# Kernel tuning notes

Hardware: AMD Instinct MI355X
Metric: run time of the kernel (lower is better)

The kernel has to match this reference:

```python
import jax, jax.numpy as jnp
import numpy as np

T, B, F_, H, D, C = 16, 1024, 512, 128, 8, 100  # trees, batch, feat, hidden, depth, classes
L = 2 ** (D + 1)  # n_leaf = 512


def _routing_tables():
    # Static per-leaf routing: node index and branch side at each depth.
    # Derived from compute_mu's gather indices:
    #   node(d, l) = 2^d - 1 + l // 2^(D+1-d);  side(d, l) = (l // 2^(D-d)) % 2
    l = np.arange(L)
    node = np.stack([(2 ** d - 1) + l // (2 ** (D + 1 - d)) for d in range(D + 1)])  # [D+1, L]
    side = np.stack([(l // (2 ** (D - d))) % 2 for d in range(D + 1)])               # [D+1, L]
    return jnp.asarray(node, dtype=jnp.int32), jnp.asarray(side.astype(np.bool_))


def setup_inputs() -> dict:
    key = jax.random.key(0)
    ks = jax.random.split(key, 4)
    return {
        "feat": jax.random.normal(ks[0], (B, F_), jnp.float32),
        "W1": jax.random.normal(ks[1], (T, F_, H), jnp.float32) * 0.05,
        "b1": jnp.zeros((T, H), jnp.float32),
        "W2": jax.random.normal(ks[2], (T, H, L), jnp.float32) * 0.05,
        "b2": jnp.zeros((T, L), jnp.float32),
        "pi": jax.random.uniform(ks[3], (T, L, C), jnp.float32, -2.0, 2.0),
    }


def reference(feat, W1, b1, W2, b2, pi):
    node, side = _routing_tables()
    # Per-tree MLP head (dropout is identity in eval mode).
    h = jax.nn.relu(jnp.einsum('bf,tfh->tbh', feat, W1) + b1[:, None, :])        # [T,B,H]
    p = jax.nn.sigmoid(jnp.einsum('tbh,thl->tbl', h, W2) + b2[:, None, :])       # [T,B,L]
    # compute_mu: product of routing probs along each root->leaf path.
    sel = p[:, :, node]                          # [T,B,D+1,L] gather (static indices)
    route = jnp.where(side, 1.0 - sel, sel)      # left -> p, right -> 1-p
    mu = jnp.prod(route, axis=2)                 # [T,B,L]
    # compute_py_x: mean over leaves then mean over trees of mu @ softmax(pi).
    leaf_p = jax.nn.softmax(pi, axis=-1)         # [T,L,C]
    py_x = jnp.einsum('tbl,tlc->bc', mu, leaf_p) / (L * T)  # [B,C]
    return jnp.log(py_x)
```

## Files before the change

### kernel.cpp

```cpp
#include <hip/hip_runtime.h>
#include <hip/hip_bf16.h>
#include <math.h>

#define T_ 16
#define B_ 1024
#define F_ 512
#define H_ 128
#define D_ 8
#define C_ 100
#define L_ 512
#define CPAD 128

typedef __attribute__((ext_vector_type(8))) short bf16x8_t;
typedef __attribute__((ext_vector_type(4))) float f32x4_t;

__device__ inline ushort f2bf(float x) {
  __hip_bfloat16 b = __float2bfloat16(x);
  return *(ushort*)&b;
}
__device__ inline float bf2f(ushort u) {
  union { unsigned int i; float f; } v;
  v.i = ((unsigned int)u) << 16;
  return v.f;
}

__global__ __launch_bounds__(256) void k_prep(
    const float* __restrict__ feat, const float* __restrict__ W1,
    const float* __restrict__ W2, const float* __restrict__ pi,
    ushort* __restrict__ feat_bf, ushort* __restrict__ W1T,
    ushort* __restrict__ W2T, ushort* __restrict__ lpT) {
  __shared__ ushort sm[8320];
  const int bid = blockIdx.x, tid = threadIdx.x;

  if (bid < 256) {
    int i = (bid * 256 + tid) * 8;
    float4 a = *(const float4*)(feat + i);
    float4 b = *(const float4*)(feat + i + 4);
    bf16x8_t o;
    o[0] = (short)f2bf(a.x); o[1] = (short)f2bf(a.y);
    o[2] = (short)f2bf(a.z); o[3] = (short)f2bf(a.w);
    o[4] = (short)f2bf(b.x); o[5] = (short)f2bf(b.y);
    o[6] = (short)f2bf(b.z); o[7] = (short)f2bf(b.w);
    *(bf16x8_t*)(feat_bf + i) = o;
    return;
  }
  if (bid < 2304) {
    float (*tile)[33] = (float(*)[33])sm;
    const float* X; ushort* XT; int K, N, kb, nb, s;
    if (bid < 1280) {
      int r = bid - 256;  kb = r & 15; nb = (r >> 4) & 3;  s = r >> 6;
      X = W1; XT = W1T; K = F_; N = H_;
    } else {
      int r = bid - 1280; kb = r & 3;  nb = (r >> 2) & 15; s = r >> 6;
      X = W2; XT = W2T; K = H_; N = L_;
    }
    const int k0 = kb * 32, n0 = nb * 32;
    const int c = tid & 31, r0 = tid >> 5;
    const float* Xs = X + (size_t)s * K * N;
    ushort* XTs = XT + (size_t)s * N * K;
#pragma unroll
    for (int j = 0; j < 4; ++j)
      tile[r0 + 8 * j][c] = Xs[(size_t)(k0 + r0 + 8 * j) * N + n0 + c];
    __syncthreads();
#pragma unroll
    for (int j = 0; j < 4; ++j)
      XTs[(size_t)(n0 + r0 + 8 * j) * K + k0 + c] = f2bf(tile[c][r0 + 8 * j]);
    return;
  }
  {
    ushort (*ts)[130] = (ushort(*)[130])sm;
    const int idx = bid - 2304;
    const int R0 = idx * 64;
    const int t = R0 >> 9, li0 = R0 & 511;
    const int wave = tid >> 6, lane = tid & 63;
    for (int it = 0; it < 16; ++it) {
      int r = wave * 16 + it;
      const float* x = pi + (size_t)(R0 + r) * C_;
      float v0 = (lane < C_) ? x[lane] : -1e30f;
      float v1 = (lane + 64 < C_) ? x[lane + 64] : -1e30f;
      float m = fmaxf(v0, v1);
#pragma unroll
      for (int off = 32; off; off >>= 1) m = fmaxf(m, __shfl_xor(m, off, 64));
      float e0 = __expf(v0 - m);
      float e1 = (lane + 64 < C_) ? __expf(v1 - m) : 0.0f;
      float s = e0 + e1;
#pragma unroll
      for (int off = 32; off; off >>= 1) s += __shfl_xor(s, off, 64);
      float inv = 1.0f / s;
      ts[r][lane]      = (lane < C_) ? f2bf(e0 * inv) : (ushort)0;
      ts[r][lane + 64] = (lane + 64 < C_) ? f2bf(e1 * inv) : (ushort)0;
    }
    __syncthreads();
    int c = tid >> 1, hf = tid & 1;
    ushort tmp[32];
#pragma unroll
    for (int j = 0; j < 32; ++j) tmp[j] = ts[hf * 32 + j][c];
    ushort* dst = lpT + ((size_t)t * CPAD + c) * L_ + li0 + hf * 32;
#pragma unroll
    for (int j = 0; j < 4; ++j)
      *(bf16x8_t*)(dst + 8 * j) = *(bf16x8_t*)&tmp[8 * j];
  }
}

__global__ __launch_bounds__(256) void k125(
    const ushort* __restrict__ feat, const ushort* __restrict__ W1T,
    const float* __restrict__ b1, const ushort* __restrict__ W2T,
    const float* __restrict__ b2, const ushort* __restrict__ lpT,
    float* __restrict__ part) {
  __shared__ ushort sm[29504];
  ushort (*a_s)[72]  = (ushort(*)[72]) sm;
  ushort (*b_s)[72]  = (ushort(*)[72])(sm + 2304);
  ushort* p_s        = sm;
  ushort (*h_s)[136] = (ushort(*)[136])(sm + 16448);
  ushort (*w_s)[136] = (ushort(*)[136])(sm + 20800);
  ushort (*lp_s)[72] = (ushort(*)[72])(sm + 16448);
  ushort (*mu_x)[72] = (ushort(*)[72])(sm + 25664);

  const int t = blockIdx.y, b0 = blockIdx.x * 32, tid = threadIdx.x;
  const int w = tid >> 6, lane = tid & 63, quad = lane >> 4, n = lane & 15;

  {
    f32x4_t acc[2][2];
#pragma unroll
    for (int i = 0; i < 2; ++i)
#pragma unroll
      for (int j = 0; j < 2; ++j) acc[i][j] = (f32x4_t){0.f, 0.f, 0.f, 0.f};

    for (int kc = 0; kc < 8; ++kc) {
      __syncthreads();
      {
        int row = tid >> 3, col8 = (tid & 7) * 8;
        *(bf16x8_t*)&a_s[row][col8] =
            *(const bf16x8_t*)(feat + (size_t)(b0 + row) * F_ + kc * 64 + col8);
      }
#pragma unroll
      for (int i = 0; i < 4; ++i) {
        int idx = i * 256 + tid;
        int row = idx >> 3, col8 = (idx & 7) * 8;
        *(bf16x8_t*)&b_s[row][col8] =
            *(const bf16x8_t*)(W1T + ((size_t)t * H_ + row) * F_ + kc * 64 + col8);
      }
      __syncthreads();
#pragma unroll
      for (int ks = 0; ks < 64; ks += 32) {
        bf16x8_t af[2], bfr[2];
#pragma unroll
        for (int mt = 0; mt < 2; ++mt)
          af[mt] = *(const bf16x8_t*)&a_s[mt * 16 + n][ks + quad * 8];
#pragma unroll
        for (int nt = 0; nt < 2; ++nt)
          bfr[nt] = *(const bf16x8_t*)&b_s[w * 32 + nt * 16 + n][ks + quad * 8];
#pragma unroll
        for (int mt = 0; mt < 2; ++mt)
#pragma unroll
          for (int nt = 0; nt < 2; ++nt)
            acc[mt][nt] = __builtin_amdgcn_mfma_f32_16x16x32_bf16(
                af[mt], bfr[nt], acc[mt][nt], 0, 0, 0);
      }
    }
    float bias[2] = {b1[t * H_ + w * 32 + n], b1[t * H_ + w * 32 + 16 + n]};
    __syncthreads();
#pragma unroll
    for (int mt = 0; mt < 2; ++mt)
#pragma unroll
      for (int nt = 0; nt < 2; ++nt)
#pragma unroll
        for (int r = 0; r < 4; ++r) {
          int row = mt * 16 + quad * 4 + r;
          int col = w * 32 + nt * 16 + n;
          float v = acc[mt][nt][r] + bias[nt];
          h_s[row][col] = f2bf(v > 0.f ? v : 0.f);
        }
  }

  for (int nc = 0; nc < 8; ++nc) {
    __syncthreads();
#pragma unroll
    for (int i = 0; i < 4; ++i) {
      int idx = i * 256 + tid;
      int row = idx >> 4, col8 = (idx & 15) * 8;
      *(bf16x8_t*)&w_s[row][col8] =
          *(const bf16x8_t*)(W2T + ((size_t)t * L_ + nc * 64 + row) * H_ + col8);
    }
    __syncthreads();
    f32x4_t acc[2];
    acc[0] = (f32x4_t){0.f, 0.f, 0.f, 0.f};
    acc[1] = (f32x4_t){0.f, 0.f, 0.f, 0.f};
#pragma unroll
    for (int ks = 0; ks < 128; ks += 32) {
      bf16x8_t bfrag = *(const bf16x8_t*)&w_s[w * 16 + n][ks + quad * 8];
#pragma unroll
      for (int mt = 0; mt < 2; ++mt) {
        bf16x8_t afrag = *(const bf16x8_t*)&h_s[mt * 16 + n][ks + quad * 8];
        acc[mt] = __builtin_amdgcn_mfma_f32_16x16x32_bf16(afrag, bfrag,
                                                          acc[mt], 0, 0, 0);
      }
    }
    int l = nc * 64 + w * 16 + n;
    float bias = b2[t * L_ + l];
#pragma unroll
    for (int mt = 0; mt < 2; ++mt)
#pragma unroll
      for (int r = 0; r < 4; ++r) {
        float x = acc[mt][r] + bias;
        p_s[(mt * 16 + quad * 4 + r) * 514 + l] = f2bf(1.0f / (1.0f + __expf(-x)));
      }
  }
  __syncthreads();

  bf16x8_t muv[4][2];
#pragma unroll
  for (int pass = 0; pass < 4; ++pass) {
    int b = pass * 8 + (tid >> 5);
    int s = tid & 31;
    float P = 1.f;
#pragma unroll
    for (int d = 0; d < 5; ++d) {
      int nd = (1 << d) - 1 + (s >> (5 - d));
      int sd = (s >> (4 - d)) & 1;
      float pv = bf2f(p_s[b * 514 + nd]);
      P *= sd ? (1.f - pv) : pv;
    }
    float p5 = bf2f(p_s[b * 514 + 31 + s]);
    float q5[2] = {P * p5, P * (1.f - p5)};
    float q6[4], q7[8];
#pragma unroll
    for (int j = 0; j < 2; ++j) {
      float pv = bf2f(p_s[b * 514 + 63 + 2 * s + j]);
      q6[2 * j] = q5[j] * pv;
      q6[2 * j + 1] = q5[j] * (1.f - pv);
    }
#pragma unroll
    for (int u = 0; u < 4; ++u) {
      float pv = bf2f(p_s[b * 514 + 127 + 4 * s + u]);
      q7[2 * u] = q6[u] * pv;
      q7[2 * u + 1] = q6[u] * (1.f - pv);
    }
    bf16x8_t o0, o1;
#pragma unroll
    for (int v = 0; v < 8; ++v) {
      float pv = bf2f(p_s[b * 514 + 255 + 8 * s + v]);
      ushort e0 = f2bf(q7[v] * pv);
      ushort e1 = f2bf(q7[v] * (1.f - pv));
      if (v < 4) { o0[2 * v] = (short)e0; o0[2 * v + 1] = (short)e1; }
      else       { o1[2 * (v - 4)] = (short)e0; o1[2 * (v - 4) + 1] = (short)e1; }
    }
    muv[pass][0] = o0;
    muv[pass][1] = o1;
  }

  f32x4_t acc[2][2];
#pragma unroll
  for (int i = 0; i < 2; ++i)
#pragma unroll
    for (int j = 0; j < 2; ++j) acc[i][j] = (f32x4_t){0.f, 0.f, 0.f, 0.f};

  const ushort* lpt_t = lpT + (size_t)t * CPAD * L_;
  for (int c = 0; c < 8; ++c) {
    {
      int row = tid >> 1, hf = tid & 1;
      const ushort* src = lpt_t + (size_t)row * L_ + c * 64 + hf * 32;
#pragma unroll
      for (int j = 0; j < 4; ++j)
        *(bf16x8_t*)&lp_s[row][hf * 32 + 8 * j] = *(const bf16x8_t*)(src + 8 * j);
    }
    if (((tid & 31) >> 2) == c) {
      int sub = tid & 3;
#pragma unroll
      for (int pass = 0; pass < 4; ++pass) {
        int b = pass * 8 + (tid >> 5);
        *(bf16x8_t*)&mu_x[b][sub * 16]     = muv[pass][0];
        *(bf16x8_t*)&mu_x[b][sub * 16 + 8] = muv[pass][1];
      }
    }
    __syncthreads();
#pragma unroll
    for (int ks = 0; ks < 64; ks += 32) {
      bf16x8_t af[2], bfr[2];
#pragma unroll
      for (int mt = 0; mt < 2; ++mt)
        af[mt] = *(const bf16x8_t*)&mu_x[mt * 16 + n][ks + quad * 8];
#pragma unroll
      for (int nt = 0; nt < 2; ++nt)
        bfr[nt] = *(const bf16x8_t*)&lp_s[w * 32 + nt * 16 + n][ks + quad * 8];
#pragma unroll
      for (int mt = 0; mt < 2; ++mt)
#pragma unroll
        for (int nt = 0; nt < 2; ++nt)
          acc[mt][nt] = __builtin_amdgcn_mfma_f32_16x16x32_bf16(
              af[mt], bfr[nt], acc[mt][nt], 0, 0, 0);
    }
    __syncthreads();
  }
#pragma unroll
  for (int mt = 0; mt < 2; ++mt)
#pragma unroll
    for (int nt = 0; nt < 2; ++nt) {
      int cc = w * 32 + nt * 16 + n;
      if (cc < C_) {
#pragma unroll
        for (int r = 0; r < 4; ++r) {
          int m = b0 + mt * 16 + quad * 4 + r;
          part[((size_t)t * B_ + m) * C_ + cc] = acc[mt][nt][r];
        }
      }
    }
}

__global__ __launch_bounds__(256) void k6_log(
    const float* __restrict__ part, float* __restrict__ out) {
  int i = blockIdx.x * 256 + threadIdx.x;
  if (i < B_ * C_) {
    float s = 0.0f;
#pragma unroll
    for (int t = 0; t < T_; ++t) s += part[(size_t)t * B_ * C_ + i];
    out[i] = logf(s * (1.0f / (L_ * T_)));
  }
}

extern "C" void kernel_launch(void* const* d_in, const int* in_sizes, int n_in,
                              void* d_out, int out_size, void* d_ws,
                              size_t ws_size, hipStream_t stream) {
  const float* feat = (const float*)d_in[0];
  const float* W1   = (const float*)d_in[1];
  const float* b1   = (const float*)d_in[2];
  const float* W2   = (const float*)d_in[3];
  const float* b2   = (const float*)d_in[4];
  const float* pi   = (const float*)d_in[5];
  float* out = (float*)d_out;

  char* ws = (char*)d_ws;
  ushort* feat_bf = (ushort*)(ws);
  ushort* W1T_buf = (ushort*)(ws + ((size_t)1 << 20));
  ushort* W2T_buf = (ushort*)(ws + ((size_t)3 << 20));
  ushort* lpT_buf = (ushort*)(ws + ((size_t)5 << 20));
  float*  part_buf = (float*)(ws + ((size_t)7 << 20));

  k_prep<<<2432, 256, 0, stream>>>(feat, W1, W2, pi, feat_bf, W1T_buf,
                                   W2T_buf, lpT_buf);
  k125<<<dim3(B_ / 32, T_), 256, 0, stream>>>(feat_bf, W1T_buf, b1, W2T_buf,
                                              b2, lpT_buf, part_buf);
  k6_log<<<(B_ * C_ + 255) / 256, 256, 0, stream>>>(part_buf, out);
}
```

Baseline: 116.9 us.

## Halve per-block batch tile to 16 rows, doubling grid and shrinking LDS

The fused MLP/routing/leaf kernel now processes 16 batch rows per block instead of 32, so the grid doubles to 1024 blocks and shared memory is re-laid out more compactly (about 41KB instead of 59KB). This targets poor occupancy and load imbalance on a GPU with many CUs, where 512 blocks leave the machine underfilled. In exchange, W1, W2 and the leaf-probability tables are reloaded from global/L2 twice as often, and each wave does half as many MFMAs per fragment load.

Result: slower. 130.6 us (+11.8%).

```diff
diff --git a/kernel.cpp b/kernel.cpp
--- a/kernel.cpp
+++ b/kernel.cpp
@@ -107,28 +107,25 @@
     const float* __restrict__ b1, const ushort* __restrict__ W2T,
     const float* __restrict__ b2, const ushort* __restrict__ lpT,
     float* __restrict__ part) {
-  __shared__ ushort sm[29504];
-  ushort (*a_s)[72]  = (ushort(*)[72]) sm;
-  ushort (*b_s)[72]  = (ushort(*)[72])(sm + 2304);
-  ushort* p_s        = sm;
-  ushort (*h_s)[136] = (ushort(*)[136])(sm + 16448);
-  ushort (*w_s)[136] = (ushort(*)[136])(sm + 20800);
-  ushort (*lp_s)[72] = (ushort(*)[72])(sm + 16448);
-  ushort (*mu_x)[72] = (ushort(*)[72])(sm + 25664);
-
-  const int t = blockIdx.y, b0 = blockIdx.x * 32, tid = threadIdx.x;
+  __shared__ ushort sm[20768];
+  ushort (*h_s)[136] = (ushort(*)[136])sm;
+  ushort* p_s        = sm + 2176;
+  ushort (*a_s)[72]  = (ushort(*)[72])(sm + 10400);
+  ushort (*b_s)[72]  = (ushort(*)[72])(sm + 11552);
+  ushort (*w_s)[136] = (ushort(*)[136])(sm + 10400);
+  ushort (*lp_s)[72] = (ushort(*)[72])sm;
+  ushort (*mu_x)[72] = (ushort(*)[72])(sm + 9216);
+
+  const int t = blockIdx.y, b0 = blockIdx.x * 16, tid = threadIdx.x;
   const int w = tid >> 6, lane = tid & 63, quad = lane >> 4, n = lane & 15;
 
   {
-    f32x4_t acc[2][2];
-#pragma unroll
-    for (int i = 0; i < 2; ++i)
-#pragma unroll
-      for (int j = 0; j < 2; ++j) acc[i][j] = (f32x4_t){0.f, 0.f, 0.f, 0.f};
-
+    f32x4_t acc[2];
+    acc[0] = (f32x4_t){0.f, 0.f, 0.f, 0.f};
+    acc[1] = (f32x4_t){0.f, 0.f, 0.f, 0.f};
     for (int kc = 0; kc < 8; ++kc) {
       __syncthreads();
-      {
+      if (tid < 128) {
         int row = tid >> 3, col8 = (tid & 7) * 8;
         *(bf16x8_t*)&a_s[row][col8] =
             *(const bf16x8_t*)(feat + (size_t)(b0 + row) * F_ + kc * 64 + col8);
@@ -143,34 +140,22 @@
       __syncthreads();
 #pragma unroll
       for (int ks = 0; ks < 64; ks += 32) {
-        bf16x8_t af[2], bfr[2];
-#pragma unroll
-        for (int mt = 0; mt < 2; ++mt)
-          af[mt] = *(const bf16x8_t*)&a_s[mt * 16 + n][ks + quad * 8];
-#pragma unroll
-        for (int nt = 0; nt < 2; ++nt)
-          bfr[nt] = *(const bf16x8_t*)&b_s[w * 32 + nt * 16 + n][ks + quad * 8];
-#pragma unroll
-        for (int mt = 0; mt < 2; ++mt)
-#pragma unroll
-          for (int nt = 0; nt < 2; ++nt)
-            acc[mt][nt] = __builtin_amdgcn_mfma_f32_16x16x32_bf16(
-                af[mt], bfr[nt], acc[mt][nt], 0, 0, 0);
+        bf16x8_t af = *(const bf16x8_t*)&a_s[n][ks + quad * 8];
+#pragma unroll
+        for (int nt = 0; nt < 2; ++nt) {
+          bf16x8_t bfr = *(const bf16x8_t*)&b_s[w * 32 + nt * 16 + n][ks + quad * 8];
+          acc[nt] = __builtin_amdgcn_mfma_f32_16x16x32_bf16(af, bfr, acc[nt], 0, 0, 0);
+        }
       }
     }
     float bias[2] = {b1[t * H_ + w * 32 + n], b1[t * H_ + w * 32 + 16 + n]};
-    __syncthreads();
-#pragma unroll
-    for (int mt = 0; mt < 2; ++mt)
-#pragma unroll
-      for (int nt = 0; nt < 2; ++nt)
-#pragma unroll
-        for (int r = 0; r < 4; ++r) {
-          int row = mt * 16 + quad * 4 + r;
-          int col = w * 32 + nt * 16 + n;
-          float v = acc[mt][nt][r] + bias[nt];
-          h_s[row][col] = f2bf(v > 0.f ? v : 0.f);
-        }
+#pragma unroll
+    for (int nt = 0; nt < 2; ++nt)
+#pragma unroll
+      for (int r = 0; r < 4; ++r) {
+        float v = acc[nt][r] + bias[nt];
+        h_s[quad * 4 + r][w * 32 + nt * 16 + n] = f2bf(v > 0.f ? v : 0.f);
+      }
   }
 
   for (int nc = 0; nc < 8; ++nc) {
@@ -183,34 +168,26 @@
           *(const bf16x8_t*)(W2T + ((size_t)t * L_ + nc * 64 + row) * H_ + col8);
     }
     __syncthreads();
-    f32x4_t acc[2];
-    acc[0] = (f32x4_t){0.f, 0.f, 0.f, 0.f};
-    acc[1] = (f32x4_t){0.f, 0.f, 0.f, 0.f};
+    f32x4_t acc = (f32x4_t){0.f, 0.f, 0.f, 0.f};
 #pragma unroll
     for (int ks = 0; ks < 128; ks += 32) {
       bf16x8_t bfrag = *(const bf16x8_t*)&w_s[w * 16 + n][ks + quad * 8];
-#pragma unroll
-      for (int mt = 0; mt < 2; ++mt) {
-        bf16x8_t afrag = *(const bf16x8_t*)&h_s[mt * 16 + n][ks + quad * 8];
-        acc[mt] = __builtin_amdgcn_mfma_f32_16x16x32_bf16(afrag, bfrag,
-                                                          acc[mt], 0, 0, 0);
-      }
+      bf16x8_t afrag = *(const bf16x8_t*)&h_s[n][ks + quad * 8];
+      acc = __builtin_amdgcn_mfma_f32_16x16x32_bf16(afrag, bfrag, acc, 0, 0, 0);
     }
     int l = nc * 64 + w * 16 + n;
     float bias = b2[t * L_ + l];
 #pragma unroll
-    for (int mt = 0; mt < 2; ++mt)
-#pragma unroll
-      for (int r = 0; r < 4; ++r) {
-        float x = acc[mt][r] + bias;
-        p_s[(mt * 16 + quad * 4 + r) * 514 + l] = f2bf(1.0f / (1.0f + __expf(-x)));
-      }
+    for (int r = 0; r < 4; ++r) {
+      float x = acc[r] + bias;
+      p_s[(quad * 4 + r) * 514 + l] = f2bf(1.0f / (1.0f + __expf(-x)));
+    }
   }
   __syncthreads();
 
-  bf16x8_t muv[4][2];
-#pragma unroll
-  for (int pass = 0; pass < 4; ++pass) {
+  bf16x8_t muv[2][2];
+#pragma unroll
+  for (int pass = 0; pass < 2; ++pass) {
     int b = pass * 8 + (tid >> 5);
     int s = tid & 31;
     float P = 1.f;
@@ -248,13 +225,11 @@
     muv[pass][0] = o0;
     muv[pass][1] = o1;
   }
-
-  f32x4_t acc[2][2];
-#pragma unroll
-  for (int i = 0; i < 2; ++i)
-#pragma unroll
-    for (int j = 0; j < 2; ++j) acc[i][j] = (f32x4_t){0.f, 0.f, 0.f, 0.f};
-
+  __syncthreads();
+
+  f32x4_t acc4[2];
+  acc4[0] = (f32x4_t){0.f, 0.f, 0.f, 0.f};
+  acc4[1] = (f32x4_t){0.f, 0.f, 0.f, 0.f};
   const ushort* lpt_t = lpT + (size_t)t * CPAD * L_;
   for (int c = 0; c < 8; ++c) {
     {
@@ -267,7 +242,7 @@
     if (((tid & 31) >> 2) == c) {
       int sub = tid & 3;
 #pragma unroll
-      for (int pass = 0; pass < 4; ++pass) {
+      for (int pass = 0; pass < 2; ++pass) {
         int b = pass * 8 + (tid >> 5);
         *(bf16x8_t*)&mu_x[b][sub * 16]     = muv[pass][0];
         *(bf16x8_t*)&mu_x[b][sub * 16 + 8] = muv[pass][1];
@@ -276,35 +251,26 @@
     __syncthreads();
 #pragma unroll
     for (int ks = 0; ks < 64; ks += 32) {
-      bf16x8_t af[2], bfr[2];
-#pragma unroll
-      for (int mt = 0; mt < 2; ++mt)
-        af[mt] = *(const bf16x8_t*)&mu_x[mt * 16 + n][ks + quad * 8];
-#pragma unroll
-      for (int nt = 0; nt < 2; ++nt)
-        bfr[nt] = *(const bf16x8_t*)&lp_s[w * 32 + nt * 16 + n][ks + quad * 8];
-#pragma unroll
-      for (int mt = 0; mt < 2; ++mt)
-#pragma unroll
-        for (int nt = 0; nt < 2; ++nt)
-          acc[mt][nt] = __builtin_amdgcn_mfma_f32_16x16x32_bf16(
-              af[mt], bfr[nt], acc[mt][nt], 0, 0, 0);
-    }
-    __syncthreads();
-  }
-#pragma unroll
-  for (int mt = 0; mt < 2; ++mt)
-#pragma unroll
-    for (int nt = 0; nt < 2; ++nt) {
-      int cc = w * 32 + nt * 16 + n;
-      if (cc < C_) {
-#pragma unroll
-        for (int r = 0; r < 4; ++r) {
-          int m = b0 + mt * 16 + quad * 4 + r;
-          part[((size_t)t * B_ + m) * C_ + cc] = acc[mt][nt][r];
-        }
-      }
-    }
+      bf16x8_t af = *(const bf16x8_t*)&mu_x[n][ks + quad * 8];
+#pragma unroll
+      for (int nt = 0; nt < 2; ++nt) {
+        bf16x8_t bfr = *(const bf16x8_t*)&lp_s[w * 32 + nt * 16 + n][ks + quad * 8];
+        acc4[nt] = __builtin_amdgcn_mfma_f32_16x16x32_bf16(af, bfr, acc4[nt], 0, 0, 0);
+      }
+    }
+    __syncthreads();
+  }
+#pragma unroll
+  for (int nt = 0; nt < 2; ++nt) {
+    int cc = w * 32 + nt * 16 + n;
+    if (cc < C_) {
+#pragma unroll
+      for (int r = 0; r < 4; ++r) {
+        int m = b0 + quad * 4 + r;
+        part[((size_t)t * B_ + m) * C_ + cc] = acc4[nt][r];
+      }
+    }
+  }
 }
 
 __global__ __launch_bounds__(256) void k6_log(
@@ -338,7 +304,7 @@
 
   k_prep<<<2432, 256, 0, stream>>>(feat, W1, W2, pi, feat_bf, W1T_buf,
                                    W2T_buf, lpT_buf);
-  k125<<<dim3(B_ / 32, T_), 256, 0, stream>>>(feat_bf, W1T_buf, b1, W2T_buf,
+  k125<<<dim3(B_ / 16, T_), 256, 0, stream>>>(feat_bf, W1T_buf, b1, W2T_buf,
                                               b2, lpT_buf, part_buf);
   k6_log<<<(B_ * C_ + 255) / 256, 256, 0, stream>>>(part_buf, out);
 }
```

## Merge prep, fused compute and log-reduce into one cooperative kernel with grid syncs

Applied to the files above, without the earlier changes.

Replaces the three kernel launches (prep, main compute, final log reduction) with a single cooperative kernel of 512 blocks. The blocks loop over the former prep work items, then meet at a grid-wide barrier before the compute phase and again before the reduction. This removes launch gaps and inter-kernel drain costs. In exchange, the prep phase runs on fewer blocks, the reduction uses 512 blocks instead of 400, the grid barriers cost time, and every block must be co-resident.

Result: slower. 366.1 us (+213.2%).

```diff
diff --git a/kernel.cpp b/kernel.cpp
--- a/kernel.cpp
+++ b/kernel.cpp
@@ -1,6 +1,9 @@
 #include <hip/hip_runtime.h>
 #include <hip/hip_bf16.h>
+#include <hip/hip_cooperative_groups.h>
 #include <math.h>
+
+namespace cg = cooperative_groups;
 
 #define T_ 16
 #define B_ 1024
@@ -10,6 +13,7 @@
 #define C_ 100
 #define L_ 512
 #define CPAD 128
+#define GRID_ 512
 
 typedef __attribute__((ext_vector_type(8))) short bf16x8_t;
 typedef __attribute__((ext_vector_type(4))) float f32x4_t;
@@ -24,121 +28,252 @@
   return v.f;
 }
 
-__global__ __launch_bounds__(256) void k_prep(
+__global__ __launch_bounds__(256) void k_all(
     const float* __restrict__ feat, const float* __restrict__ W1,
-    const float* __restrict__ W2, const float* __restrict__ pi,
+    const float* __restrict__ b1, const float* __restrict__ W2,
+    const float* __restrict__ b2, const float* __restrict__ pi,
     ushort* __restrict__ feat_bf, ushort* __restrict__ W1T,
-    ushort* __restrict__ W2T, ushort* __restrict__ lpT) {
-  __shared__ ushort sm[8320];
+    ushort* __restrict__ W2T, ushort* __restrict__ lpT,
+    float* __restrict__ part, float* __restrict__ out) {
+  __shared__ ushort sm[29504];
   const int bid = blockIdx.x, tid = threadIdx.x;
 
-  if (bid < 256) {
-    int i = (bid * 256 + tid) * 8;
-    float4 a = *(const float4*)(feat + i);
-    float4 b = *(const float4*)(feat + i + 4);
-    bf16x8_t o;
-    o[0] = (short)f2bf(a.x); o[1] = (short)f2bf(a.y);
-    o[2] = (short)f2bf(a.z); o[3] = (short)f2bf(a.w);
-    o[4] = (short)f2bf(b.x); o[5] = (short)f2bf(b.y);
-    o[6] = (short)f2bf(b.z); o[7] = (short)f2bf(b.w);
-    *(bf16x8_t*)(feat_bf + i) = o;
-    return;
+  for (int u = bid; u < 2432; u += GRID_) {
+    if (u < 256) {
+      int i = (u * 256 + tid) * 8;
+      float4 a = *(const float4*)(feat + i);
+      float4 b = *(const float4*)(feat + i + 4);
+      bf16x8_t o;
+      o[0] = (short)f2bf(a.x); o[1] = (short)f2bf(a.y);
+      o[2] = (short)f2bf(a.z); o[3] = (short)f2bf(a.w);
+      o[4] = (short)f2bf(b.x); o[5] = (short)f2bf(b.y);
+      o[6] = (short)f2bf(b.z); o[7] = (short)f2bf(b.w);
+      *(bf16x8_t*)(feat_bf + i) = o;
+    } else if (u < 2304) {
+      __syncthreads();
+      float (*tile)[33] = (float(*)[33])sm;
+      const float* X; ushort* XT; int K, N, kb, nb, s;
+      if (u < 1280) {
+        int r = u - 256;  kb = r & 15; nb = (r >> 4) & 3;  s = r >> 6;
+        X = W1; XT = W1T; K = F_; N = H_;
+      } else {
+        int r = u - 1280; kb = r & 3;  nb = (r >> 2) & 15; s = r >> 6;
+        X = W2; XT = W2T; K = H_; N = L_;
+      }
+      const int k0 = kb * 32, n0 = nb * 32;
+      const int c = tid & 31, r0 = tid >> 5;
+      const float* Xs = X + (size_t)s * K * N;
+      ushort* XTs = XT + (size_t)s * N * K;
+#pragma unroll
+      for (int j = 0; j < 4; ++j)
+        tile[r0 + 8 * j][c] = Xs[(size_t)(k0 + r0 + 8 * j) * N + n0 + c];
+      __syncthreads();
+#pragma unroll
+      for (int j = 0; j < 4; ++j)
+        XTs[(size_t)(n0 + r0 + 8 * j) * K + k0 + c] = f2bf(tile[c][r0 + 8 * j]);
+    } else {
+      __syncthreads();
+      ushort (*ts)[130] = (ushort(*)[130])sm;
+      const int idx = u - 2304;
+      const int R0 = idx * 64;
+      const int t = R0 >> 9, li0 = R0 & 511;
+      const int wave = tid >> 6, lane = tid & 63;
+      for (int it = 0; it < 16; ++it) {
+        int r = wave * 16 + it;
+        const float* x = pi + (size_t)(R0 + r) * C_;
+        float v0 = (lane < C_) ? x[lane] : -1e30f;
+        float v1 = (lane + 64 < C_) ? x[lane + 64] : -1e30f;
+        float m = fmaxf(v0, v1);
+#pragma unroll
+        for (int off = 32; off; off >>= 1) m = fmaxf(m, __shfl_xor(m, off, 64));
+        float e0 = __expf(v0 - m);
+        float e1 = (lane + 64 < C_) ? __expf(v1 - m) : 0.0f;
+        float s = e0 + e1;
+#pragma unroll
+        for (int off = 32; off; off >>= 1) s += __shfl_xor(s, off, 64);
+        float inv = 1.0f / s;
+        ts[r][lane]      = (lane < C_) ? f2bf(e0 * inv) : (ushort)0;
+        ts[r][lane + 64] = (lane + 64 < C_) ? f2bf(e1 * inv) : (ushort)0;
+      }
+      __syncthreads();
+      int c = tid >> 1, hf = tid & 1;
+      ushort tmp[32];
+#pragma unroll
+      for (int j = 0; j < 32; ++j) tmp[j] = ts[hf * 32 + j][c];
+      ushort* dst = lpT + ((size_t)t * CPAD + c) * L_ + li0 + hf * 32;
+#pragma unroll
+      for (int j = 0; j < 4; ++j)
+        *(bf16x8_t*)(dst + 8 * j) = *(bf16x8_t*)&tmp[8 * j];
+    }
   }
-  if (bid < 2304) {
-    float (*tile)[33] = (float(*)[33])sm;
-    const float* X; ushort* XT; int K, N, kb, nb, s;
-    if (bid < 1280) {
-      int r = bid - 256;  kb = r & 15; nb = (r >> 4) & 3;  s = r >> 6;
-      X = W1; XT = W1T; K = F_; N = H_;
-    } else {
-      int r = bid - 1280; kb = r & 3;  nb = (r >> 2) & 15; s = r >> 6;
-      X = W2; XT = W2T; K = H_; N = L_;
-    }
-    const int k0 = kb * 32, n0 = nb * 32;
-    const int c = tid & 31, r0 = tid >> 5;
-    const float* Xs = X + (size_t)s * K * N;
-    ushort* XTs = XT + (size_t)s * N * K;
-#pragma unroll
-    for (int j = 0; j < 4; ++j)
-      tile[r0 + 8 * j][c] = Xs[(size_t)(k0 + r0 + 8 * j) * N + n0 + c];
-    __syncthreads();
-#pragma unroll
-    for (int j = 0; j < 4; ++j)
-      XTs[(size_t)(n0 + r0 + 8 * j) * K + k0 + c] = f2bf(tile[c][r0 + 8 * j]);
-    return;
-  }
+  __threadfence();
+  cg::this_grid().sync();
+
   {
-    ushort (*ts)[130] = (ushort(*)[130])sm;
-    const int idx = bid - 2304;
-    const int R0 = idx * 64;
-    const int t = R0 >> 9, li0 = R0 & 511;
-    const int wave = tid >> 6, lane = tid & 63;
-    for (int it = 0; it < 16; ++it) {
-      int r = wave * 16 + it;
-      const float* x = pi + (size_t)(R0 + r) * C_;
-      float v0 = (lane < C_) ? x[lane] : -1e30f;
-      float v1 = (lane + 64 < C_) ? x[lane + 64] : -1e30f;
-      float m = fmaxf(v0, v1);
-#pragma unroll
-      for (int off = 32; off; off >>= 1) m = fmaxf(m, __shfl_xor(m, off, 64));
-      float e0 = __expf(v0 - m);
-      float e1 = (lane + 64 < C_) ? __expf(v1 - m) : 0.0f;
-      float s = e0 + e1;
-#pragma unroll
-      for (int off = 32; off; off >>= 1) s += __shfl_xor(s, off, 64);
-      float inv = 1.0f / s;
-      ts[r][lane]      = (lane < C_) ? f2bf(e0 * inv) : (ushort)0;
-      ts[r][lane + 64] = (lane + 64 < C_) ? f2bf(e1 * inv) : (ushort)0;
-    }
-    __syncthreads();
-    int c = tid >> 1, hf = tid & 1;
-    ushort tmp[32];
-#pragma unroll
-    for (int j = 0; j < 32; ++j) tmp[j] = ts[hf * 32 + j][c];
-    ushort* dst = lpT + ((size_t)t * CPAD + c) * L_ + li0 + hf * 32;
-#pragma unroll
-    for (int j = 0; j < 4; ++j)
-      *(bf16x8_t*)(dst + 8 * j) = *(bf16x8_t*)&tmp[8 * j];
-  }
-}
-
-__global__ __launch_bounds__(256) void k125(
-    const ushort* __restrict__ feat, const ushort* __restrict__ W1T,
-    const float* __restrict__ b1, const ushort* __restrict__ W2T,
-    const float* __restrict__ b2, const ushort* __restrict__ lpT,
-    float* __restrict__ part) {
-  __shared__ ushort sm[29504];
-  ushort (*a_s)[72]  = (ushort(*)[72]) sm;
-  ushort (*b_s)[72]  = (ushort(*)[72])(sm + 2304);
-  ushort* p_s        = sm;
-  ushort (*h_s)[136] = (ushort(*)[136])(sm + 16448);
-  ushort (*w_s)[136] = (ushort(*)[136])(sm + 20800);
-  ushort (*lp_s)[72] = (ushort(*)[72])(sm + 16448);
-  ushort (*mu_x)[72] = (ushort(*)[72])(sm + 25664);
-
-  const int t = blockIdx.y, b0 = blockIdx.x * 32, tid = threadIdx.x;
-  const int w = tid >> 6, lane = tid & 63, quad = lane >> 4, n = lane & 15;
-
-  {
-    f32x4_t acc[2][2];
-#pragma unroll
-    for (int i = 0; i < 2; ++i)
-#pragma unroll
-      for (int j = 0; j < 2; ++j) acc[i][j] = (f32x4_t){0.f, 0.f, 0.f, 0.f};
-
-    for (int kc = 0; kc < 8; ++kc) {
-      __syncthreads();
-      {
-        int row = tid >> 3, col8 = (tid & 7) * 8;
-        *(bf16x8_t*)&a_s[row][col8] =
-            *(const bf16x8_t*)(feat + (size_t)(b0 + row) * F_ + kc * 64 + col8);
-      }
+    ushort (*a_s)[72]  = (ushort(*)[72]) sm;
+    ushort (*b_s)[72]  = (ushort(*)[72])(sm + 2304);
+    ushort* p_s        = sm;
+    ushort (*h_s)[136] = (ushort(*)[136])(sm + 16448);
+    ushort (*w_s)[136] = (ushort(*)[136])(sm + 20800);
+    ushort (*lp_s)[72] = (ushort(*)[72])(sm + 16448);
+    ushort (*mu_x)[72] = (ushort(*)[72])(sm + 25664);
+
+    const int t = bid >> 5, b0 = (bid & 31) * 32;
+    const int w = tid >> 6, lane = tid & 63, quad = lane >> 4, n = lane & 15;
+
+    {
+      f32x4_t acc[2][2];
+#pragma unroll
+      for (int i = 0; i < 2; ++i)
+#pragma unroll
+        for (int j = 0; j < 2; ++j) acc[i][j] = (f32x4_t){0.f, 0.f, 0.f, 0.f};
+
+      for (int kc = 0; kc < 8; ++kc) {
+        __syncthreads();
+        {
+          int row = tid >> 3, col8 = (tid & 7) * 8;
+          *(bf16x8_t*)&a_s[row][col8] =
+              *(const bf16x8_t*)(feat_bf + (size_t)(b0 + row) * F_ + kc * 64 + col8);
+        }
+#pragma unroll
+        for (int i = 0; i < 4; ++i) {
+          int idx = i * 256 + tid;
+          int row = idx >> 3, col8 = (idx & 7) * 8;
+          *(bf16x8_t*)&b_s[row][col8] =
+              *(const bf16x8_t*)(W1T + ((size_t)t * H_ + row) * F_ + kc * 64 + col8);
+        }
+        __syncthreads();
+#pragma unroll
+        for (int ks = 0; ks < 64; ks += 32) {
+          bf16x8_t af[2], bfr[2];
+#pragma unroll
+          for (int mt = 0; mt < 2; ++mt)
+            af[mt] = *(const bf16x8_t*)&a_s[mt * 16 + n][ks + quad * 8];
+#pragma unroll
+          for (int nt = 0; nt < 2; ++nt)
+            bfr[nt] = *(const bf16x8_t*)&b_s[w * 32 + nt * 16 + n][ks + quad * 8];
+#pragma unroll
+          for (int mt = 0; mt < 2; ++mt)
+#pragma unroll
+            for (int nt = 0; nt < 2; ++nt)
+              acc[mt][nt] = __builtin_amdgcn_mfma_f32_16x16x32_bf16(
+                  af[mt], bfr[nt], acc[mt][nt], 0, 0, 0);
+        }
+      }
+      float bias[2] = {b1[t * H_ + w * 32 + n], b1[t * H_ + w * 32 + 16 + n]};
+      __syncthreads();
+#pragma unroll
+      for (int mt = 0; mt < 2; ++mt)
+#pragma unroll
+        for (int nt = 0; nt < 2; ++nt)
+#pragma unroll
+          for (int r = 0; r < 4; ++r) {
+            int row = mt * 16 + quad * 4 + r;
+            int col = w * 32 + nt * 16 + n;
+            float v = acc[mt][nt][r] + bias[nt];
+            h_s[row][col] = f2bf(v > 0.f ? v : 0.f);
+          }
+    }
+
+    for (int nc = 0; nc < 8; ++nc) {
+      __syncthreads();
 #pragma unroll
       for (int i = 0; i < 4; ++i) {
         int idx = i * 256 + tid;
-        int row = idx >> 3, col8 = (idx & 7) * 8;
-        *(bf16x8_t*)&b_s[row][col8] =
-            *(const bf16x8_t*)(W1T + ((size_t)t * H_ + row) * F_ + kc * 64 + col8);
+        int row = idx >> 4, col8 = (idx & 15) * 8;
+        *(bf16x8_t*)&w_s[row][col8] =
+            *(const bf16x8_t*)(W2T + ((size_t)t * L_ + nc * 64 + row) * H_ + col8);
+      }
+      __syncthreads();
+      f32x4_t acc[2];
+      acc[0] = (f32x4_t){0.f, 0.f, 0.f, 0.f};
+      acc[1] = (f32x4_t){0.f, 0.f, 0.f, 0.f};
+#pragma unroll
+      for (int ks = 0; ks < 128; ks += 32) {
+        bf16x8_t bfrag = *(const bf16x8_t*)&w_s[w * 16 + n][ks + quad * 8];
+#pragma unroll
+        for (int mt = 0; mt < 2; ++mt) {
+          bf16x8_t afrag = *(const bf16x8_t*)&h_s[mt * 16 + n][ks + quad * 8];
+          acc[mt] = __builtin_amdgcn_mfma_f32_16x16x32_bf16(afrag, bfrag,
+                                                            acc[mt], 0, 0, 0);
+        }
+      }
+      int l = nc * 64 + w * 16 + n;
+      float bias = b2[t * L_ + l];
+#pragma unroll
+      for (int mt = 0; mt < 2; ++mt)
+#pragma unroll
+        for (int r = 0; r < 4; ++r) {
+          float x = acc[mt][r] + bias;
+          p_s[(mt * 16 + quad * 4 + r) * 514 + l] = f2bf(1.0f / (1.0f + __expf(-x)));
+        }
+    }
+    __syncthreads();
+
+    bf16x8_t muv[4][2];
+#pragma unroll
+    for (int pass = 0; pass < 4; ++pass) {
+      int b = pass * 8 + (tid >> 5);
+      int s = tid & 31;
+      float P = 1.f;
+#pragma unroll
+      for (int d = 0; d < 5; ++d) {
+        int nd = (1 << d) - 1 + (s >> (5 - d));
+        int sd = (s >> (4 - d)) & 1;
+        float pv = bf2f(p_s[b * 514 + nd]);
+        P *= sd ? (1.f - pv) : pv;
+      }
+      float p5 = bf2f(p_s[b * 514 + 31 + s]);
+      float q5[2] = {P * p5, P * (1.f - p5)};
+      float q6[4], q7[8];
+#pragma unroll
+      for (int j = 0; j < 2; ++j) {
+        float pv = bf2f(p_s[b * 514 + 63 + 2 * s + j]);
+        q6[2 * j] = q5[j] * pv;
+        q6[2 * j + 1] = q5[j] * (1.f - pv);
+      }
+#pragma unroll
+      for (int uu = 0; uu < 4; ++uu) {
+        float pv = bf2f(p_s[b * 514 + 127 + 4 * s + uu]);
+        q7[2 * uu] = q6[uu] * pv;
+        q7[2 * uu + 1] = q6[uu] * (1.f - pv);
+      }
+      bf16x8_t o0, o1;
+#pragma unroll
+      for (int v = 0; v < 8; ++v) {
+        float pv = bf2f(p_s[b * 514 + 255 + 8 * s + v]);
+        ushort e0 = f2bf(q7[v] * pv);
+        ushort e1 = f2bf(q7[v] * (1.f - pv));
+        if (v < 4) { o0[2 * v] = (short)e0; o0[2 * v + 1] = (short)e1; }
+        else       { o1[2 * (v - 4)] = (short)e0; o1[2 * (v - 4) + 1] = (short)e1; }
+      }
+      muv[pass][0] = o0;
+      muv[pass][1] = o1;
+    }
+
+    f32x4_t acc4[2][2];
+#pragma unroll
+    for (int i = 0; i < 2; ++i)
+#pragma unroll
+      for (int j = 0; j < 2; ++j) acc4[i][j] = (f32x4_t){0.f, 0.f, 0.f, 0.f};
+
+    const ushort* lpt_t = lpT + (size_t)t * CPAD * L_;
+    for (int c = 0; c < 8; ++c) {
+      {
+        int row = tid >> 1, hf = tid & 1;
+        const ushort* src = lpt_t + (size_t)row * L_ + c * 64 + hf * 32;
+#pragma unroll
+        for (int j = 0; j < 4; ++j)
+          *(bf16x8_t*)&lp_s[row][hf * 32 + 8 * j] = *(const bf16x8_t*)(src + 8 * j);
+      }
+      if (((tid & 31) >> 2) == c) {
+        int sub = tid & 3;
+#pragma unroll
+        for (int pass = 0; pass < 4; ++pass) {
+          int b = pass * 8 + (tid >> 5);
+          *(bf16x8_t*)&mu_x[b][sub * 16]     = muv[pass][0];
+          *(bf16x8_t*)&mu_x[b][sub * 16 + 8] = muv[pass][1];
+        }
       }
       __syncthreads();
 #pragma unroll
@@ -146,175 +281,44 @@
         bf16x8_t af[2], bfr[2];
 #pragma unroll
         for (int mt = 0; mt < 2; ++mt)
-          af[mt] = *(const bf16x8_t*)&a_s[mt * 16 + n][ks + quad * 8];
+          af[mt] = *(const bf16x8_t*)&mu_x[mt * 16 + n][ks + quad * 8];
 #pragma unroll
         for (int nt = 0; nt < 2; ++nt)
-          bfr[nt] = *(const bf16x8_t*)&b_s[w * 32 + nt * 16 + n][ks + quad * 8];
+          bfr[nt] = *(const bf16x8_t*)&lp_s[w * 32 + nt * 16 + n][ks + quad * 8];
 #pragma unroll
         for (int mt = 0; mt < 2; ++mt)
 #pragma unroll
           for (int nt = 0; nt < 2; ++nt)
-            acc[mt][nt] = __builtin_amdgcn_mfma_f32_16x16x32_bf16(
-                af[mt], bfr[nt], acc[mt][nt], 0, 0, 0);
-      }
-    }
-    float bias[2] = {b1[t * H_ + w * 32 + n], b1[t * H_ + w * 32 + 16 + n]};
-    __syncthreads();
+            acc4[mt][nt] = __builtin_amdgcn_mfma_f32_16x16x32_bf16(
+                af[mt], bfr[nt], acc4[mt][nt], 0, 0, 0);
+      }
+      __syncthreads();
+    }
 #pragma unroll
     for (int mt = 0; mt < 2; ++mt)
 #pragma unroll
-      for (int nt = 0; nt < 2; ++nt)
-#pragma unroll
-        for (int r = 0; r < 4; ++r) {
-          int row = mt * 16 + quad * 4 + r;
-          int col = w * 32 + nt * 16 + n;
-          float v = acc[mt][nt][r] + bias[nt];
-          h_s[row][col] = f2bf(v > 0.f ? v : 0.f);
-        }
+      for (int nt = 0; nt < 2; ++nt) {
+        int cc = w * 32 + nt * 16 + n;
+        if (cc < C_) {
+#pragma unroll
+          for (int r = 0; r < 4; ++r) {
+            int m = b0 + mt * 16 + quad * 4 + r;
+            part[((size_t)t * B_ + m) * C_ + cc] = acc4[mt][nt][r];
+          }
+        }
+      }
   }
-
-  for (int nc = 0; nc < 8; ++nc) {
-    __syncthreads();
-#pragma unroll
-    for (int i = 0; i < 4; ++i) {
-      int idx = i * 256 + tid;
-      int row = idx >> 4, col8 = (idx & 15) * 8;
-      *(bf16x8_t*)&w_s[row][col8] =
-          *(const bf16x8_t*)(W2T + ((size_t)t * L_ + nc * 64 + row) * H_ + col8);
-    }
-    __syncthreads();
-    f32x4_t acc[2];
-    acc[0] = (f32x4_t){0.f, 0.f, 0.f, 0.f};
-    acc[1] = (f32x4_t){0.f, 0.f, 0.f, 0.f};
-#pragma unroll
-    for (int ks = 0; ks < 128; ks += 32) {
-      bf16x8_t bfrag = *(const bf16x8_t*)&w_s[w * 16 + n][ks + quad * 8];
-#pragma unroll
-      for (int mt = 0; mt < 2; ++mt) {
-        bf16x8_t afrag = *(const bf16x8_t*)&h_s[mt * 16 + n][ks + quad * 8];
-        acc[mt] = __builtin_amdgcn_mfma_f32_16x16x32_bf16(afrag, bfrag,
-                                                          acc[mt], 0, 0, 0);
-      }
-    }
-    int l = nc * 64 + w * 16 + n;
-    float bias = b2[t * L_ + l];
-#pragma unroll
-    for (int mt = 0; mt < 2; ++mt)
-#pragma unroll
-      for (int r = 0; r < 4; ++r) {
-        float x = acc[mt][r] + bias;
-        p_s[(mt * 16 + quad * 4 + r) * 514 + l] = f2bf(1.0f / (1.0f + __expf(-x)));
-      }
-  }
-  __syncthreads();
-
-  bf16x8_t muv[4][2];
-#pragma unroll
-  for (int pass = 0; pass < 4; ++pass) {
-    int b = pass * 8 + (tid >> 5);
-    int s = tid & 31;
-    float P = 1.f;
-#pragma unroll
-    for (int d = 0; d < 5; ++d) {
-      int nd = (1 << d) - 1 + (s >> (5 - d));
-      int sd = (s >> (4 - d)) & 1;
-      float pv = bf2f(p_s[b * 514 + nd]);
-      P *= sd ? (1.f - pv) : pv;
-    }
-    float p5 = bf2f(p_s[b * 514 + 31 + s]);
-    float q5[2] = {P * p5, P * (1.f - p5)};
-    float q6[4], q7[8];
-#pragma unroll
-    for (int j = 0; j < 2; ++j) {
-      float pv = bf2f(p_s[b * 514 + 63 + 2 * s + j]);
-      q6[2 * j] = q5[j] * pv;
-      q6[2 * j + 1] = q5[j] * (1.f - pv);
-    }
-#pragma unroll
-    for (int u = 0; u < 4; ++u) {
-      float pv = bf2f(p_s[b * 514 + 127 + 4 * s + u]);
-      q7[2 * u] = q6[u] * pv;
-      q7[2 * u + 1] = q6[u] * (1.f - pv);
-    }
-    bf16x8_t o0, o1;
-#pragma unroll
-    for (int v = 0; v < 8; ++v) {
-      float pv = bf2f(p_s[b * 514 + 255 + 8 * s + v]);
-      ushort e0 = f2bf(q7[v] * pv);
-      ushort e1 = f2bf(q7[v] * (1.f - pv));
-      if (v < 4) { o0[2 * v] = (short)e0; o0[2 * v + 1] = (short)e1; }
-      else       { o1[2 * (v - 4)] = (short)e0; o1[2 * (v - 4) + 1] = (short)e1; }
-    }
-    muv[pass][0] = o0;
-    muv[pass][1] = o1;
-  }
-
-  f32x4_t acc[2][2];
-#pragma unroll
-  for (int i = 0; i < 2; ++i)
-#pragma unroll
-    for (int j = 0; j < 2; ++j) acc[i][j] = (f32x4_t){0.f, 0.f, 0.f, 0.f};
-
-  const ushort* lpt_t = lpT + (size_t)t * CPAD * L_;
-  for (int c = 0; c < 8; ++c) {
-    {
-      int row = tid >> 1, hf = tid & 1;
-      const ushort* src = lpt_t + (size_t)row * L_ + c * 64 + hf * 32;
-#pragma unroll
-      for (int j = 0; j < 4; ++j)
-        *(bf16x8_t*)&lp_s[row][hf * 32 + 8 * j] = *(const bf16x8_t*)(src + 8 * j);
-    }
-    if (((tid & 31) >> 2) == c) {
-      int sub = tid & 3;
-#pragma unroll
-      for (int pass = 0; pass < 4; ++pass) {
-        int b = pass * 8 + (tid >> 5);
-        *(bf16x8_t*)&mu_x[b][sub * 16]     = muv[pass][0];
-        *(bf16x8_t*)&mu_x[b][sub * 16 + 8] = muv[pass][1];
-      }
-    }
-    __syncthreads();
-#pragma unroll
-    for (int ks = 0; ks < 64; ks += 32) {
-      bf16x8_t af[2], bfr[2];
-#pragma unroll
-      for (int mt = 0; mt < 2; ++mt)
-        af[mt] = *(const bf16x8_t*)&mu_x[mt * 16 + n][ks + quad * 8];
-#pragma unroll
-      for (int nt = 0; nt < 2; ++nt)
-        bfr[nt] = *(const bf16x8_t*)&lp_s[w * 32 + nt * 16 + n][ks + quad * 8];
-#pragma unroll
-      for (int mt = 0; mt < 2; ++mt)
-#pragma unroll
-        for (int nt = 0; nt < 2; ++nt)
-          acc[mt][nt] = __builtin_amdgcn_mfma_f32_16x16x32_bf16(
-              af[mt], bfr[nt], acc[mt][nt], 0, 0, 0);
-    }
-    __syncthreads();
-  }
-#pragma unroll
-  for (int mt = 0; mt < 2; ++mt)
-#pragma unroll
-    for (int nt = 0; nt < 2; ++nt) {
-      int cc = w * 32 + nt * 16 + n;
-      if (cc < C_) {
-#pragma unroll
-        for (int r = 0; r < 4; ++r) {
-          int m = b0 + mt * 16 + quad * 4 + r;
-          part[((size_t)t * B_ + m) * C_ + cc] = acc[mt][nt][r];
-        }
-      }
-    }
-}
-
-__global__ __launch_bounds__(256) void k6_log(
-    const float* __restrict__ part, float* __restrict__ out) {
-  int i = blockIdx.x * 256 + threadIdx.x;
-  if (i < B_ * C_) {
-    float s = 0.0f;
-#pragma unroll
-    for (int t = 0; t < T_; ++t) s += part[(size_t)t * B_ * C_ + i];
-    out[i] = logf(s * (1.0f / (L_ * T_)));
+  __threadfence();
+  cg::this_grid().sync();
+
+  {
+    int i = bid * 256 + tid;
+    if (i < B_ * C_) {
+      float s = 0.0f;
+#pragma unroll
+      for (int t = 0; t < T_; ++t) s += part[(size_t)t * B_ * C_ + i];
+      out[i] = logf(s * (1.0f / (L_ * T_)));
+    }
   }
 }
 
@@ -336,9 +340,10 @@
   ushort* lpT_buf = (ushort*)(ws + ((size_t)5 << 20));
   float*  part_buf = (float*)(ws + ((size_t)7 << 20));
 
-  k_prep<<<2432, 256, 0, stream>>>(feat, W1, W2, pi, feat_bf, W1T_buf,
-                                   W2T_buf, lpT_buf);
-  k125<<<dim3(B_ / 32, T_), 256, 0, stream>>>(feat_bf, W1T_buf, b1, W2T_buf,
-                                              b2, lpT_buf, part_buf);
-  k6_log<<<(B_ * C_ + 255) / 256, 256, 0, stream>>>(part_buf, out);
+  void* args[] = {
+      (void*)&feat, (void*)&W1, (void*)&b1, (void*)&W2, (void*)&b2,
+      (void*)&pi,   (void*)&feat_bf, (void*)&W1T_buf, (void*)&W2T_buf,
+      (void*)&lpT_buf, (void*)&part_buf, (void*)&out};
+  hipLaunchCooperativeKernel((const void*)k_all, dim3(GRID_), dim3(256),
+                             args, 0, stream);
 }
```

## Split fused MLP+routing kernel from leaf matmul via global mu buffer

Applied to the files above, without the earlier changes.

The fused kernel that computed the MLP, routing products and the mu×softmax(pi) matmul is split in two. The first kernel writes mu in bf16 to a 16 MB workspace buffer, and the second kernel reads mu fragments straight from global memory to feed MFMA. This is meant to lower shared-memory and register pressure and remove the staged mu register-to-LDS shuffle. The cost is an extra kernel launch and a global round-trip for mu.

After: 124.8 us. 6.8% more time.

```diff
diff --git a/kernel.cpp b/kernel.cpp
--- a/kernel.cpp
+++ b/kernel.cpp
@@ -102,19 +102,16 @@
   }
 }
 
-__global__ __launch_bounds__(256) void k125(
+__global__ __launch_bounds__(256) void k12_mfma(
     const ushort* __restrict__ feat, const ushort* __restrict__ W1T,
     const float* __restrict__ b1, const ushort* __restrict__ W2T,
-    const float* __restrict__ b2, const ushort* __restrict__ lpT,
-    float* __restrict__ part) {
-  __shared__ ushort sm[29504];
-  ushort (*a_s)[72]  = (ushort(*)[72]) sm;
-  ushort (*b_s)[72]  = (ushort(*)[72])(sm + 2304);
-  ushort* p_s        = sm;
-  ushort (*h_s)[136] = (ushort(*)[136])(sm + 16448);
-  ushort (*w_s)[136] = (ushort(*)[136])(sm + 20800);
-  ushort (*lp_s)[72] = (ushort(*)[72])(sm + 16448);
-  ushort (*mu_x)[72] = (ushort(*)[72])(sm + 25664);
+    const float* __restrict__ b2, ushort* __restrict__ mu) {
+  __shared__ ushort smem[29696];
+  ushort (*h_s)[136] = (ushort(*)[136])smem;
+  ushort (*a_s)[72]  = (ushort(*)[72])(smem + 4352);
+  ushort (*b_s)[72]  = (ushort(*)[72])(smem + 6656);
+  ushort (*w_s)[136] = (ushort(*)[136])(smem + 4352);
+  ushort (*p_s)[520] = (ushort(*)[520])(smem + 13056);
 
   const int t = blockIdx.y, b0 = blockIdx.x * 32, tid = threadIdx.x;
   const int w = tid >> 6, lane = tid & 63, quad = lane >> 4, n = lane & 15;
@@ -203,12 +200,11 @@
 #pragma unroll
       for (int r = 0; r < 4; ++r) {
         float x = acc[mt][r] + bias;
-        p_s[(mt * 16 + quad * 4 + r) * 514 + l] = f2bf(1.0f / (1.0f + __expf(-x)));
+        p_s[mt * 16 + quad * 4 + r][l] = f2bf(1.0f / (1.0f + __expf(-x)));
       }
   }
   __syncthreads();
 
-  bf16x8_t muv[4][2];
 #pragma unroll
   for (int pass = 0; pass < 4; ++pass) {
     int b = pass * 8 + (tid >> 5);
@@ -218,36 +214,45 @@
     for (int d = 0; d < 5; ++d) {
       int nd = (1 << d) - 1 + (s >> (5 - d));
       int sd = (s >> (4 - d)) & 1;
-      float pv = bf2f(p_s[b * 514 + nd]);
+      float pv = bf2f(p_s[b][nd]);
       P *= sd ? (1.f - pv) : pv;
     }
-    float p5 = bf2f(p_s[b * 514 + 31 + s]);
+    float p5 = bf2f(p_s[b][31 + s]);
     float q5[2] = {P * p5, P * (1.f - p5)};
     float q6[4], q7[8];
 #pragma unroll
     for (int j = 0; j < 2; ++j) {
-      float pv = bf2f(p_s[b * 514 + 63 + 2 * s + j]);
+      float pv = bf2f(p_s[b][63 + 2 * s + j]);
       q6[2 * j] = q5[j] * pv;
       q6[2 * j + 1] = q5[j] * (1.f - pv);
     }
 #pragma unroll
     for (int u = 0; u < 4; ++u) {
-      float pv = bf2f(p_s[b * 514 + 127 + 4 * s + u]);
+      float pv = bf2f(p_s[b][127 + 4 * s + u]);
       q7[2 * u] = q6[u] * pv;
       q7[2 * u + 1] = q6[u] * (1.f - pv);
     }
     bf16x8_t o0, o1;
 #pragma unroll
     for (int v = 0; v < 8; ++v) {
-      float pv = bf2f(p_s[b * 514 + 255 + 8 * s + v]);
+      float pv = bf2f(p_s[b][255 + 8 * s + v]);
       ushort e0 = f2bf(q7[v] * pv);
       ushort e1 = f2bf(q7[v] * (1.f - pv));
       if (v < 4) { o0[2 * v] = (short)e0; o0[2 * v + 1] = (short)e1; }
       else       { o1[2 * (v - 4)] = (short)e0; o1[2 * (v - 4) + 1] = (short)e1; }
     }
-    muv[pass][0] = o0;
-    muv[pass][1] = o1;
-  }
+    ushort* dst = mu + ((size_t)t * B_ + b0 + b) * L_ + s * 16;
+    *(bf16x8_t*)dst = o0;
+    *(bf16x8_t*)(dst + 8) = o1;
+  }
+}
+
+__global__ __launch_bounds__(256) void k5_mfma(
+    const ushort* __restrict__ mu, const ushort* __restrict__ lpT,
+    float* __restrict__ part) {
+  __shared__ ushort lp_s[CPAD][72];
+  const int t = blockIdx.y, m0 = blockIdx.x * 32, tid = threadIdx.x;
+  const int w = tid >> 6, lane = tid & 63, quad = lane >> 4, n = lane & 15;
 
   f32x4_t acc[2][2];
 #pragma unroll
@@ -255,8 +260,11 @@
 #pragma unroll
     for (int j = 0; j < 2; ++j) acc[i][j] = (f32x4_t){0.f, 0.f, 0.f, 0.f};
 
-  const ushort* lpt_t = lpT + (size_t)t * CPAD * L_;
+  const ushort* lpt_t  = lpT + (size_t)t * CPAD * L_;
+  const ushort* muBase = mu + ((size_t)t * B_ + m0) * L_;
+
   for (int c = 0; c < 8; ++c) {
+    __syncthreads();
     {
       int row = tid >> 1, hf = tid & 1;
       const ushort* src = lpt_t + (size_t)row * L_ + c * 64 + hf * 32;
@@ -264,22 +272,14 @@
       for (int j = 0; j < 4; ++j)
         *(bf16x8_t*)&lp_s[row][hf * 32 + 8 * j] = *(const bf16x8_t*)(src + 8 * j);
     }
-    if (((tid & 31) >> 2) == c) {
-      int sub = tid & 3;
-#pragma unroll
-      for (int pass = 0; pass < 4; ++pass) {
-        int b = pass * 8 + (tid >> 5);
-        *(bf16x8_t*)&mu_x[b][sub * 16]     = muv[pass][0];
-        *(bf16x8_t*)&mu_x[b][sub * 16 + 8] = muv[pass][1];
-      }
-    }
     __syncthreads();
 #pragma unroll
     for (int ks = 0; ks < 64; ks += 32) {
       bf16x8_t af[2], bfr[2];
 #pragma unroll
       for (int mt = 0; mt < 2; ++mt)
-        af[mt] = *(const bf16x8_t*)&mu_x[mt * 16 + n][ks + quad * 8];
+        af[mt] = *(const bf16x8_t*)(muBase + (size_t)(mt * 16 + n) * L_ +
+                                    c * 64 + ks + quad * 8);
 #pragma unroll
       for (int nt = 0; nt < 2; ++nt)
         bfr[nt] = *(const bf16x8_t*)&lp_s[w * 32 + nt * 16 + n][ks + quad * 8];
@@ -290,7 +290,6 @@
           acc[mt][nt] = __builtin_amdgcn_mfma_f32_16x16x32_bf16(
               af[mt], bfr[nt], acc[mt][nt], 0, 0, 0);
     }
-    __syncthreads();
   }
 #pragma unroll
   for (int mt = 0; mt < 2; ++mt)
@@ -300,7 +299,7 @@
       if (cc < C_) {
 #pragma unroll
         for (int r = 0; r < 4; ++r) {
-          int m = b0 + mt * 16 + quad * 4 + r;
+          int m = m0 + mt * 16 + quad * 4 + r;
           part[((size_t)t * B_ + m) * C_ + cc] = acc[mt][nt][r];
         }
       }
@@ -334,11 +333,13 @@
   ushort* W1T_buf = (ushort*)(ws + ((size_t)1 << 20));
   ushort* W2T_buf = (ushort*)(ws + ((size_t)3 << 20));
   ushort* lpT_buf = (ushort*)(ws + ((size_t)5 << 20));
-  float*  part_buf = (float*)(ws + ((size_t)7 << 20));
+  ushort* mu_buf  = (ushort*)(ws + ((size_t)7 << 20));
+  float*  part_buf = (float*)(ws + ((size_t)23 << 20));
 
   k_prep<<<2432, 256, 0, stream>>>(feat, W1, W2, pi, feat_bf, W1T_buf,
                                    W2T_buf, lpT_buf);
-  k125<<<dim3(B_ / 32, T_), 256, 0, stream>>>(feat_bf, W1T_buf, b1, W2T_buf,
-                                              b2, lpT_buf, part_buf);
+  k12_mfma<<<dim3(B_ / 32, T_), 256, 0, stream>>>(feat_bf, W1T_buf, b1,
+                                                  W2T_buf, b2, mu_buf);
+  k5_mfma<<<dim3(B_ / 32, T_), 256, 0, stream>>>(mu_buf, lpT_buf, part_buf);
   k6_log<<<(B_ * C_ + 255) / 256, 256, 0, stream>>>(part_buf, out);
 }
```
